# Kernel tuning notes

Measured on AMD Instinct MI355X. Metric: run time of the kernel, lower is better.

## Reference

```python
import jax, jax.numpy as jnp
import numpy as np

LN_EPS = 1e-5


def _layer_norm(x, g, b):
    mu = x.mean(-1, keepdims=True)
    var = ((x - mu) ** 2).mean(-1, keepdims=True)
    return (x - mu) / jnp.sqrt(var + LN_EPS) * g + b


def _process_memory(mem, mem_W, mem_b, ln_g, ln_b):
    # deep memory MLP: Linear -> LayerNorm -> SiLU per layer (dropout = identity in eval)
    h = mem
    for i in range(mem_W.shape[0]):
        h = jax.nn.silu(_layer_norm(h @ mem_W[i] + mem_b[i], ln_g[i], ln_b[i]))
    return h


def setup_inputs() -> dict:
    key = jax.random.key(0)
    B, S, D, M, L = 32, 2048, 1024, 1024, 2
    ks = jax.random.split(key, 12)
    s = 0.02
    inp = {
        'inputs': jax.random.normal(ks[0], (B, S, D), dtype=jnp.float32),
        'memory_state': jnp.zeros((B, M), dtype=jnp.float32),
        'momentum_state': jnp.zeros((B, M), dtype=jnp.float32),
        # projections (stored [in, out], equivalent to torch Linear weight.T)
        'Wk': jax.random.normal(ks[1], (D, M)) * s, 'bk': jnp.zeros((M,)),
        'Wv': jax.random.normal(ks[2], (D, M)) * s, 'bv': jnp.zeros((M,)),
        # deep memory layers, stacked over num_layers
        'mem_W': jax.random.normal(ks[3], (L, M, M)) * s,
        'mem_b': jnp.zeros((L, M)),
        'ln_g': jnp.ones((L, M)),
        'ln_b': jnp.zeros((L, M)),
        # gates: in = D + M
        'Wf': jax.random.normal(ks[4], (D + M, M)) * s, 'bf': jnp.zeros((M,)),
        'Wm': jax.random.normal(ks[5], (D + M, M)) * s, 'bm': jnp.zeros((M,)),
        'Wu': jax.random.normal(ks[6], (D + M, M)) * s, 'bu': jnp.zeros((M,)),
        'eta': jnp.ones((1,)) * 0.9,
        'theta': jnp.ones((1,)) * 0.1,
    }
    return inp


def reference(inputs, memory_state, momentum_state, Wk, bk, Wv, bv,
              mem_W, mem_b, ln_g, ln_b, Wf, bf, Wm, bm, Wu, bu, eta, theta):
    keys = inputs @ Wk + bk      # [B,S,M]
    values = inputs @ Wv + bv    # [B,S,M]

    def assoc_loss(mem):
        mo = _process_memory(mem, mem_W, mem_b, ln_g, ln_b)      # [B,M]
        pred = jnp.einsum('bsm,bm->bs', keys, mo)                # bmm(keys, mo^T)
        diff = pred[..., None] - values                          # expand to [B,S,M]
        return 0.5 * jnp.mean(diff ** 2)

    surprise_grad = jax.grad(assoc_loss)(memory_state)           # [B,M]

    pooled = inputs.mean(axis=1)                                 # [B,D]
    gate_in = jnp.concatenate([pooled, memory_state], axis=-1)   # [B,D+M]
    forget_g = jax.nn.sigmoid(gate_in @ Wf + bf)
    update_g = jax.nn.sigmoid(gate_in @ Wu + bu)
    # momentum_gate computed in source but unused in the update
    _ = jax.nn.sigmoid(gate_in @ Wm + bm)

    new_momentum = eta * momentum_state + theta * surprise_grad
    new_memory = (1.0 - forget_g) * memory_state + update_g * new_momentum

    processed = _process_memory(new_memory, mem_W, mem_b, ln_g, ln_b)
    return processed, jax.lax.stop_gradient(new_memory)
```

## Files before the change

kernel.cpp:

```cpp
#include <hip/hip_runtime.h>
#include <math.h>

#define Bc 32
#define Sc 2048
#define Dc 1024
#define Mc 1024
#define LNEPS 1e-5f
#define SCv (1.f/67108864.f)

typedef float f32x4 __attribute__((ext_vector_type(4)));

__device__ __forceinline__ float4 f4add(float4 a, float4 b) {
    return make_float4(a.x + b.x, a.y + b.y, a.z + b.z, a.w + b.w);
}

__device__ __forceinline__ void dreduce(float& a, float& b, float* sm) {
#pragma unroll
    for (int o = 32; o; o >>= 1) { a += __shfl_xor(a, o); b += __shfl_xor(b, o); }
    int w = threadIdx.x >> 6;
    if ((threadIdx.x & 63) == 0) { sm[w] = a; sm[4 + w] = b; }
    __syncthreads();
    a = sm[0] + sm[1] + sm[2] + sm[3];
    b = sm[4] + sm[5] + sm[6] + sm[7];
    __syncthreads();
}

__device__ __forceinline__ void wreduce(float& a, float& b) {
#pragma unroll
    for (int o = 32; o; o >>= 1) { a += __shfl_xor(a, o); b += __shfl_xor(b, o); }
}

__device__ __forceinline__ void nt_map(int t, int& n0i, int& b0i, int& ks) {
    int xcd = t & 7, rest = t >> 3;
    b0i = rest & 3;
    int q = rest >> 2;
    int s = q * 8 + xcd;
    ks = s >> 4; n0i = s & 15;
}
__device__ __forceinline__ void t_map(int t, int& dc, int& b, int& mc) {
    int xcd = t & 7, rest = t >> 3;
    b = rest & 31;
    int q = rest >> 5;
    int s = q * 8 + xcd;
    dc = s >> 3; mc = s & 7;
}

__device__ __forceinline__ void load_A128(float* Atile, const float* A, int b0, int k0) {
    for (int i = threadIdx.x; i < 1024; i += 256) {
        int r = i >> 7, c = i & 127;
        Atile[i] = A[(size_t)(b0 + r) * 1024 + k0 + c];
    }
}

__device__ __forceinline__ void nt_inner128v(const float* Atile, const float* W, int k0, int n0,
                                             float* P, int ks, int b0) {
    int lane = threadIdx.x & 63, bl = threadIdx.x >> 6;
    int n4 = lane & 15, kg = lane >> 4;
    const float* a0 = Atile + bl * 128;
    const float* a1 = Atile + (bl + 4) * 128;
    const float4* Wp = (const float4*)(W + (size_t)k0 * 1024 + n0);
    float4 acc0 = make_float4(0.f, 0.f, 0.f, 0.f);
    float4 acc1 = make_float4(0.f, 0.f, 0.f, 0.f);
#pragma unroll 8
    for (int i = 0; i < 32; ++i) {
        int k = i * 4 + kg;
        float4 w4 = Wp[(size_t)k * 256 + n4];
        float av0 = a0[k], av1 = a1[k];
        acc0.x = fmaf(av0, w4.x, acc0.x); acc0.y = fmaf(av0, w4.y, acc0.y);
        acc0.z = fmaf(av0, w4.z, acc0.z); acc0.w = fmaf(av0, w4.w, acc0.w);
        acc1.x = fmaf(av1, w4.x, acc1.x); acc1.y = fmaf(av1, w4.y, acc1.y);
        acc1.z = fmaf(av1, w4.z, acc1.z); acc1.w = fmaf(av1, w4.w, acc1.w);
    }
#pragma unroll
    for (int o = 16; o <= 32; o <<= 1) {
        acc0.x += __shfl_xor(acc0.x, o); acc0.y += __shfl_xor(acc0.y, o);
        acc0.z += __shfl_xor(acc0.z, o); acc0.w += __shfl_xor(acc0.w, o);
        acc1.x += __shfl_xor(acc1.x, o); acc1.y += __shfl_xor(acc1.y, o);
        acc1.z += __shfl_xor(acc1.z, o); acc1.w += __shfl_xor(acc1.w, o);
    }
    if (kg == 0) {
        size_t base = (size_t)ks * 32768 + n0 + 4 * n4;
        *(float4*)&P[base + (size_t)(b0 + bl) * 1024] = acc0;
        *(float4*)&P[base + (size_t)(b0 + bl + 4) * 1024] = acc1;
    }
}

__device__ __forceinline__ void t_inner(const float* Asl, const float* W,
                                        int dbase, int m0, float* outp) {
    int lane = threadIdx.x & 63, wv = threadIdx.x >> 6;
    int half = lane >> 5, m4 = lane & 31;
    float4 a4 = ((const float4*)Asl)[m4];
    int d0 = dbase + wv * 64 + half;
    float res = 0.f;
#pragma unroll 8
    for (int p = 0; p < 32; ++p) {
        int d = d0 + p * 2;
        float4 w4 = ((const float4*)(W + (size_t)d * 1024 + m0))[m4];
        float v = w4.x * a4.x + w4.y * a4.y + w4.z * a4.z + w4.w * a4.w;
#pragma unroll
        for (int o = 1; o < 32; o <<= 1) v += __shfl_xor(v, o);
        res = (m4 == p) ? v : res;
    }
    outp[wv * 64 + m4 * 2 + half] = res;
}

__global__ __launch_bounds__(256) void k_front(const float* __restrict__ Wv, const float* __restrict__ bv,
                        const float* __restrict__ mem, const float* __restrict__ W0,
                        float* __restrict__ wv_row, float* __restrict__ bvsum,
                        float* __restrict__ P1a) {
    __shared__ float shm[1032];
    int bid = blockIdx.x, tid = threadIdx.x;
    if (bid < 256) {
        float s1 = 0.f, s2 = 0.f, s3 = 0.f, s4 = 0.f;
        for (int m = tid; m < 1024; m += 256) {
            s1 += Wv[(size_t)bid * 1024 + m];
            s2 += Wv[(size_t)(bid + 256) * 1024 + m];
            s3 += Wv[(size_t)(bid + 512) * 1024 + m];
            s4 += Wv[(size_t)(bid + 768) * 1024 + m];
        }
        dreduce(s1, s2, shm + 1024);
        dreduce(s3, s4, shm + 1024);
        if (tid == 0) {
            wv_row[bid] = s1; wv_row[bid + 256] = s2;
            wv_row[bid + 512] = s3; wv_row[bid + 768] = s4;
        }
        if (bid == 0) {
            float v = 0.f, d2 = 0.f;
            for (int m = tid; m < 1024; m += 256) v += bv[m];
            dreduce(v, d2, shm + 1024);
            if (tid == 0) *bvsum = v;
        }
    } else {
        int n0i, b0i, ks;
        nt_map(bid - 256, n0i, b0i, ks);
        int n0 = n0i * 64, b0 = b0i * 8, k0 = ks * 128;
        load_A128(shm, mem, b0, k0);
        __syncthreads();
        nt_inner128v(shm, W0, k0, n0, P1a, ks, b0);
    }
}

__global__ __launch_bounds__(256) void k_gemm_ln(const float* __restrict__ P, const float* __restrict__ bias,
                          const float* __restrict__ g, const float* __restrict__ be,
                          const float* __restrict__ W1, float* __restrict__ Pout) {
    __shared__ float shm[1040];
    int tid = threadIdx.x;
    int n0i, b0i, ks;
    nt_map(blockIdx.x, n0i, b0i, ks);
    int n0 = n0i * 64, b0 = b0i * 8, k0 = ks * 128;
    float* Atile = shm; float* stats = shm + 1024;
    int wv = tid >> 6, lane = tid & 63;
    const float4* b4 = (const float4*)bias;
    for (int rr = 0; rr < 2; ++rr) {
        int r = wv + rr * 4, b = b0 + r;
        float s = 0.f, sq = 0.f;
#pragma unroll
        for (int q = 0; q < 4; ++q) {
            int m4 = lane + 64 * q;
            float4 z4 = b4[m4];
#pragma unroll
            for (int k2 = 0; k2 < 8; ++k2) {
                float4 v = ((const float4*)(P + (size_t)k2 * 32768 + (size_t)b * 1024))[m4];
                z4 = f4add(z4, v);
            }
            int c0 = 4 * m4 - k0;
            if ((unsigned)c0 < 128u) *(float4*)(Atile + r * 128 + c0) = z4;
            s += z4.x + z4.y + z4.z + z4.w;
            sq += z4.x * z4.x + z4.y * z4.y + z4.z * z4.z + z4.w * z4.w;
        }
        wreduce(s, sq);
        if (lane == 0) {
            float mean = s * (1.f / 1024.f);
            stats[r] = mean;
            stats[8 + r] = rsqrtf(sq * (1.f / 1024.f) - mean * mean + LNEPS);
        }
    }
    __syncthreads();
    for (int i = tid; i < 1024; i += 256) {
        int r = i >> 7, c = i & 127, m = k0 + c;
        float xh = (Atile[i] - stats[r]) * stats[8 + r];
        float y = fmaf(xh, g[m], be[m]);
        float sg = 1.f / (1.f + __expf(-y));
        Atile[i] = y * sg;
    }
    __syncthreads();
    nt_inner128v(Atile, W1, k0, n0, Pout, ks, b0);
}

__global__ __launch_bounds__(256) void k_wpart(const float* __restrict__ P2a, const float* __restrict__ memb1,
                        const float* __restrict__ lng1, const float* __restrict__ lnb1,
                        const float* __restrict__ bk, const float* __restrict__ Wk,
                        float* __restrict__ wpart, float* __restrict__ cbpart) {
    __shared__ float shm[136];
    int tid = threadIdx.x;
    int dc, b, mc;
    t_map(blockIdx.x, dc, b, mc);
    int m0 = mc * 128;
    float* red = shm + 128;
    float4 z4 = ((const float4*)memb1)[tid];
#pragma unroll
    for (int k2 = 0; k2 < 8; ++k2) {
        float4 v = ((const float4*)(P2a + (size_t)k2 * 32768 + (size_t)b * 1024))[tid];
        z4 = f4add(z4, v);
    }
    float s = z4.x + z4.y + z4.z + z4.w;
    float sq = z4.x * z4.x + z4.y * z4.y + z4.z * z4.z + z4.w * z4.w;
    int c0 = 4 * tid - m0;
    if ((unsigned)c0 < 128u) *(float4*)(shm + c0) = z4;
    dreduce(s, sq, red);
    float mean = s * (1.f / 1024.f);
    float rstd = rsqrtf(sq * (1.f / 1024.f) - mean * mean + LNEPS);
    if (tid < 128) {
        int m = m0 + tid;
        float xh = (shm[tid] - mean) * rstd;
        float y = fmaf(xh, lng1[m], lnb1[m]);
        float sg = 1.f / (1.f + __expf(-y));
        shm[tid] = y * sg;
    }
    __syncthreads();
    if (dc == 0) {
        float c = (tid < 128) ? bk[m0 + tid] * shm[tid] : 0.f;
        float d2 = 0.f;
        dreduce(c, d2, red);
        if (tid == 0) cbpart[mc * 32 + b] = c;
    }
    t_inner(shm, Wk, dc * 256, m0, wpart + (size_t)(mc * 32 + b) * 1024 + dc * 256);
}

__global__ __launch_bounds__(256) void k_bigpass(const float* __restrict__ X, const float* __restrict__ wpart,
                          const float* __restrict__ wv_row, const float* __restrict__ cbpart,
                          const float* __restrict__ bvsum,
                          float* __restrict__ t_part, float* __restrict__ p_part,
                          float* __restrict__ rs_part) {
    __shared__ float red[4][1024];
    __shared__ float rsum_s[4];
    int b = blockIdx.y, ch = blockIdx.x;
    int wv = threadIdx.x >> 6, lane = threadIdx.x & 63;
    float4 wreg[4], tacc[4], pacc[4];
    const float4* wp4 = (const float4*)wpart;
    const float4* wr4 = (const float4*)wv_row;
#pragma unroll
    for (int j = 0; j < 4; ++j) {
        int d4 = lane + 64 * j;
        float4 a = make_float4(0.f, 0.f, 0.f, 0.f);
#pragma unroll
        for (int mc = 0; mc < 8; ++mc) a = f4add(a, wp4[(size_t)(mc * 32 + b) * 256 + d4]);
        float4 wr = wr4[d4];
        wreg[j].x = 1024.f * a.x - wr.x;
        wreg[j].y = 1024.f * a.y - wr.y;
        wreg[j].z = 1024.f * a.z - wr.z;
        wreg[j].w = 1024.f * a.w - wr.w;
        tacc[j] = make_float4(0.f, 0.f, 0.f, 0.f);
        pacc[j] = make_float4(0.f, 0.f, 0.f, 0.f);
    }
    float cbs = 0.f;
#pragma unroll
    for (int mc = 0; mc < 8; ++mc) cbs += cbpart[mc * 32 + b];
    float cbv = 1024.f * cbs - *bvsum;
    float rloc = 0.f;
    int s0r = ch * 64 + wv * 16;
#pragma unroll 2
    for (int i = 0; i < 16; ++i) {
        const f32x4* xr = (const f32x4*)(X + ((size_t)b * Sc + s0r + i) * Dc);
        f32x4 x[4]; float pp = 0.f;
#pragma unroll
        for (int j = 0; j < 4; ++j) {
            x[j] = __builtin_nontemporal_load(xr + lane + 64 * j);
            pp += x[j].x * wreg[j].x + x[j].y * wreg[j].y + x[j].z * wreg[j].z + x[j].w * wreg[j].w;
        }
#pragma unroll
        for (int o = 32; o; o >>= 1) pp += __shfl_xor(pp, o);
        float r = pp + cbv;
        rloc += r;
#pragma unroll
        for (int j = 0; j < 4; ++j) {
            tacc[j].x = fmaf(x[j].x, r, tacc[j].x);
            tacc[j].y = fmaf(x[j].y, r, tacc[j].y);
            tacc[j].z = fmaf(x[j].z, r, tacc[j].z);
            tacc[j].w = fmaf(x[j].w, r, tacc[j].w);
            pacc[j].x += x[j].x; pacc[j].y += x[j].y;
            pacc[j].z += x[j].z; pacc[j].w += x[j].w;
        }
    }
    float4* redv = (float4*)red[wv];
#pragma unroll
    for (int j = 0; j < 4; ++j) redv[lane + 64 * j] = tacc[j];
    if (lane == 0) rsum_s[wv] = rloc;
    __syncthreads();
    size_t pb = ((size_t)b * 32 + ch) * 1024;
    for (int j = 0; j < 4; ++j) {
        int d = threadIdx.x + 256 * j;
        t_part[pb + d] = red[0][d] + red[1][d] + red[2][d] + red[3][d];
    }
    if (threadIdx.x == 0) rs_part[b * 32 + ch] = rsum_s[0] + rsum_s[1] + rsum_s[2] + rsum_s[3];
    __syncthreads();
#pragma unroll
    for (int j = 0; j < 4; ++j) redv[lane + 64 * j] = pacc[j];
    __syncthreads();
    for (int j = 0; j < 4; ++j) {
        int d = threadIdx.x + 256 * j;
        p_part[pb + d] = red[0][d] + red[1][d] + red[2][d] + red[3][d];
    }
}

__global__ __launch_bounds__(256) void k_reduce(const float* __restrict__ t_part, const float* __restrict__ p_part,
                         const float* __restrict__ rs_part,
                         float* __restrict__ tbuf, float* __restrict__ pooled,
                         float* __restrict__ rsv) {
    int idx = blockIdx.x * 256 + threadIdx.x;
    int b = idx >> 8, d4 = idx & 255;
    const float4* tp = (const float4*)t_part + (size_t)b * 8192 + d4;
    const float4* pp = (const float4*)p_part + (size_t)b * 8192 + d4;
    float4 st = make_float4(0.f, 0.f, 0.f, 0.f);
    float4 sp = make_float4(0.f, 0.f, 0.f, 0.f);
#pragma unroll 8
    for (int ch = 0; ch < 32; ++ch) {
        st = f4add(st, tp[(size_t)ch * 256]);
        sp = f4add(sp, pp[(size_t)ch * 256]);
    }
    ((float4*)tbuf)[idx] = st;
    sp.x *= (1.f / 2048.f); sp.y *= (1.f / 2048.f);
    sp.z *= (1.f / 2048.f); sp.w *= (1.f / 2048.f);
    ((float4*)pooled)[idx] = sp;
    if (blockIdx.x == 0 && threadIdx.x < 32) {
        float s = 0.f;
        for (int ch = 0; ch < 32; ++ch) s += rs_part[threadIdx.x * 32 + ch];
        rsv[threadIdx.x] = s;
    }
}

__global__ __launch_bounds__(256) void k_gates(const float* __restrict__ tbuf, const float* __restrict__ pooled,
                        const float* __restrict__ mem,
                        const float* __restrict__ Wk, const float* __restrict__ Wf,
                        const float* __restrict__ Wu,
                        float* __restrict__ Pg, float* __restrict__ Pfp, float* __restrict__ Pup,
                        float* __restrict__ Pfm, float* __restrict__ Pum) {
    __shared__ float Atile[1024];
    int bid = blockIdx.x;
    int z = bid >> 9;
    int n0i, b0i, ks;
    nt_map(bid & 511, n0i, b0i, ks);
    int n0 = n0i * 64, b0 = b0i * 8, k0 = ks * 128;
    const float* A; const float* W; float* P;
    if (z == 0)      { A = tbuf;   W = Wk;                          P = Pg; }
    else if (z == 1) { A = pooled; W = Wf;                          P = Pfp; }
    else if (z == 2) { A = pooled; W = Wu;                          P = Pup; }
    else if (z == 3) { A = mem;    W = Wf + (size_t)1024 * 1024;    P = Pfm; }
    else             { A = mem;    W = Wu + (size_t)1024 * 1024;    P = Pum; }
    load_A128(Atile, A, b0, k0);
    __syncthreads();
    nt_inner128v(Atile, W, k0, n0, P, ks, b0);
}

__global__ __launch_bounds__(256) void k_lnbwd_gemmT(const float* __restrict__ Pz, const float* __restrict__ bias,
                              const float* __restrict__ g, const float* __restrict__ be,
                              const float* __restrict__ Pgrad, int mode,
                              const float* __restrict__ bk, const float* __restrict__ rsv,
                              const float* __restrict__ W, float* __restrict__ Pout) {
    __shared__ float shm[392];
    int tid = threadIdx.x;
    int dc, b, mc;
    t_map(blockIdx.x, dc, b, mc);
    int m0 = mc * 128;
    float* red = shm + 384;
    float rsb = mode ? rsv[b] : 0.f;
    float4 z4 = ((const float4*)bias)[tid];
#pragma unroll
    for (int k2 = 0; k2 < 8; ++k2) {
        float4 v = ((const float4*)(Pz + (size_t)k2 * 32768 + (size_t)b * 1024))[tid];
        z4 = f4add(z4, v);
    }
    float s = z4.x + z4.y + z4.z + z4.w;
    float sq = z4.x * z4.x + z4.y * z4.y + z4.z * z4.z + z4.w * z4.w;
    dreduce(s, sq, red);
    float mean = s * (1.f / 1024.f);
    float rstd = rsqrtf(sq * (1.f / 1024.f) - mean * mean + LNEPS);
    float4 g4 = make_float4(0.f, 0.f, 0.f, 0.f);
#pragma unroll
    for (int k2 = 0; k2 < 8; ++k2) {
        float4 v = ((const float4*)(Pgrad + (size_t)k2 * 32768 + (size_t)b * 1024))[tid];
        g4 = f4add(g4, v);
    }
    if (mode) {
        float4 bk4 = ((const float4*)bk)[tid];
        g4.x = SCv * (g4.x + bk4.x * rsb);
        g4.y = SCv * (g4.y + bk4.y * rsb);
        g4.z = SCv * (g4.z + bk4.z * rsb);
        g4.w = SCv * (g4.w + bk4.w * rsb);
    }
    float4 gg = ((const float4*)g)[tid], bb = ((const float4*)be)[tid];
    float sa = 0.f, sax = 0.f;
    float4 a4, xh4;
    {
        xh4.x = (z4.x - mean) * rstd;
        float y = fmaf(xh4.x, gg.x, bb.x);
        float sg2 = 1.f / (1.f + __expf(-y));
        a4.x = g4.x * (sg2 * (1.f + y * (1.f - sg2))) * gg.x;
        sa += a4.x; sax += a4.x * xh4.x;
        xh4.y = (z4.y - mean) * rstd;
        y = fmaf(xh4.y, gg.y, bb.y);
        sg2 = 1.f / (1.f + __expf(-y));
        a4.y = g4.y * (sg2 * (1.f + y * (1.f - sg2))) * gg.y;
        sa += a4.y; sax += a4.y * xh4.y;
        xh4.z = (z4.z - mean) * rstd;
        y = fmaf(xh4.z, gg.z, bb.z);
        sg2 = 1.f / (1.f + __expf(-y));
        a4.z = g4.z * (sg2 * (1.f + y * (1.f - sg2))) * gg.z;
        sa += a4.z; sax += a4.z * xh4.z;
        xh4.w = (z4.w - mean) * rstd;
        y = fmaf(xh4.w, gg.w, bb.w);
        sg2 = 1.f / (1.f + __expf(-y));
        a4.w = g4.w * (sg2 * (1.f + y * (1.f - sg2))) * gg.w;
        sa += a4.w; sax += a4.w * xh4.w;
    }
    int c0 = 4 * tid - m0;
    if ((unsigned)c0 < 128u) {
        *(float4*)(shm + c0) = a4;
        *(float4*)(shm + 128 + c0) = xh4;
    }
    dreduce(sa, sax, red);
    float ma = sa * (1.f / 1024.f), mx = sax * (1.f / 1024.f);
    if (tid < 128) shm[256 + tid] = rstd * (shm[tid] - ma - shm[128 + tid] * mx);
    __syncthreads();
    t_inner(shm + 256, W, dc * 256, m0, Pout + (size_t)(mc * 32 + b) * 1024 + dc * 256);
}

__global__ __launch_bounds__(256) void k_upd_g3(const float* __restrict__ Pfm, const float* __restrict__ Pfp,
                         const float* __restrict__ Pum, const float* __restrict__ Pup,
                         const float* __restrict__ surp,
                         const float* __restrict__ bf, const float* __restrict__ bu,
                         const float* __restrict__ mem, const float* __restrict__ mom,
                         const float* __restrict__ eta, const float* __restrict__ theta,
                         const float* __restrict__ W0, float* __restrict__ P3a,
                         float* __restrict__ out_nm) {
    __shared__ float Atile[1024];
    int tid = threadIdx.x;
    int n0i, b0i, ks;
    nt_map(blockIdx.x, n0i, b0i, ks);
    int n0 = n0i * 64, b0 = b0i * 8, k0 = ks * 128;
    float etav = eta[0], thv = theta[0];
    int r = tid >> 5, c4 = tid & 31, b = b0 + r;
    int m4 = (k0 >> 2) + c4;
    float4 zf = ((const float4*)bf)[m4];
    float4 zu = ((const float4*)bu)[m4];
    float4 sv = make_float4(0.f, 0.f, 0.f, 0.f);
#pragma unroll
    for (int k2 = 0; k2 < 8; ++k2) {
        size_t ob4 = (size_t)k2 * 8192 + (size_t)b * 256 + m4;
        zf = f4add(zf, f4add(((const float4*)Pfm)[ob4], ((const float4*)Pfp)[ob4]));
        zu = f4add(zu, f4add(((const float4*)Pum)[ob4], ((const float4*)Pup)[ob4]));
        sv = f4add(sv, ((const float4*)surp)[ob4]);
    }
    float4 me = ((const float4*)mem)[(size_t)b * 256 + m4];
    float4 mo = ((const float4*)mom)[(size_t)b * 256 + m4];
    float4 nm;
    {
        float f = 1.f / (1.f + __expf(-zf.x)), u = 1.f / (1.f + __expf(-zu.x));
        nm.x = (1.f - f) * me.x + u * (etav * mo.x + thv * sv.x);
        f = 1.f / (1.f + __expf(-zf.y)); u = 1.f / (1.f + __expf(-zu.y));
        nm.y = (1.f - f) * me.y + u * (etav * mo.y + thv * sv.y);
        f = 1.f / (1.f + __expf(-zf.z)); u = 1.f / (1.f + __expf(-zu.z));
        nm.z = (1.f - f) * me.z + u * (etav * mo.z + thv * sv.z);
        f = 1.f / (1.f + __expf(-zf.w)); u = 1.f / (1.f + __expf(-zu.w));
        nm.w = (1.f - f) * me.w + u * (etav * mo.w + thv * sv.w);
    }
    *(float4*)(Atile + r * 128 + 4 * c4) = nm;
    if (n0i == 0) ((float4*)out_nm)[(size_t)b * 256 + m4] = nm;
    __syncthreads();
    nt_inner128v(Atile, W0, k0, n0, P3a, ks, b0);
}

__global__ __launch_bounds__(256) void k_final(const float* __restrict__ P4a, const float* __restrict__ memb1,
                        const float* __restrict__ lng1, const float* __restrict__ lnb1,
                        float* __restrict__ out) {
    __shared__ float sm[8];
    int b = blockIdx.x, tid = threadIdx.x;
    float4 z4 = ((const float4*)memb1)[tid];
#pragma unroll
    for (int k2 = 0; k2 < 8; ++k2) {
        float4 v = ((const float4*)(P4a + (size_t)k2 * 32768 + (size_t)b * 1024))[tid];
        z4 = f4add(z4, v);
    }
    float s = z4.x + z4.y + z4.z + z4.w;
    float sq = z4.x * z4.x + z4.y * z4.y + z4.z * z4.z + z4.w * z4.w;
    dreduce(s, sq, sm);
    float mean = s * (1.f / 1024.f);
    float rstd = rsqrtf(sq * (1.f / 1024.f) - mean * mean + LNEPS);
    float4 gg = ((const float4*)lng1)[tid], bb = ((const float4*)lnb1)[tid];
    float4 o;
    {
        float xh = (z4.x - mean) * rstd, y = fmaf(xh, gg.x, bb.x);
        o.x = y / (1.f + __expf(-y));
        xh = (z4.y - mean) * rstd; y = fmaf(xh, gg.y, bb.y);
        o.y = y / (1.f + __expf(-y));
        xh = (z4.z - mean) * rstd; y = fmaf(xh, gg.z, bb.z);
        o.z = y / (1.f + __expf(-y));
        xh = (z4.w - mean) * rstd; y = fmaf(xh, gg.w, bb.w);
        o.w = y / (1.f + __expf(-y));
    }
    ((float4*)out)[(size_t)b * 256 + tid] = o;
}

extern "C" void kernel_launch(void* const* d_in, const int* in_sizes, int n_in,
                              void* d_out, int out_size, void* d_ws, size_t ws_size,
                              hipStream_t stream) {
    const float* X    = (const float*)d_in[0];
    const float* mem  = (const float*)d_in[1];
    const float* mom  = (const float*)d_in[2];
    const float* Wk   = (const float*)d_in[3];
    const float* bk   = (const float*)d_in[4];
    const float* Wv   = (const float*)d_in[5];
    const float* bv   = (const float*)d_in[6];
    const float* memW = (const float*)d_in[7];
    const float* memb = (const float*)d_in[8];
    const float* lng  = (const float*)d_in[9];
    const float* lnb  = (const float*)d_in[10];
    const float* Wf   = (const float*)d_in[11];
    const float* bf   = (const float*)d_in[12];
    const float* Wu   = (const float*)d_in[15];
    const float* bu   = (const float*)d_in[16];
    const float* eta  = (const float*)d_in[17];
    const float* theta= (const float*)d_in[18];
    float* out = (float*)d_out;

    const size_t BM = (size_t)Bc * Mc;
    float* ws = (float*)d_ws;
    float* P1a    = ws;
    float* P2a    = ws + 8 * BM;
    float* wpart  = ws + 16 * BM;
    float* Pg     = ws + 24 * BM;
    float* Pfp    = ws + 32 * BM;
    float* Pup    = ws + 40 * BM;
    float* Pfm    = ws + 48 * BM;
    float* Pum    = ws + 56 * BM;
    float* ghp    = ws + 64 * BM;
    float* surp   = ws + 72 * BM;
    float* P3a    = ws + 80 * BM;
    float* P4a    = ws + 88 * BM;
    float* t_part = ws + 96 * BM;
    float* p_part = ws + 128 * BM;
    float* tbuf   = ws + 160 * BM;
    float* pooled = ws + 161 * BM;
    float* wv_row = ws + 162 * BM;
    float* bvsum  = wv_row + 1024;
    float* cbpart = bvsum + 1;
    float* rs_part= cbpart + 256;
    float* rsv    = rs_part + 1024;

    const float* W0 = memW;
    const float* W1 = memW + (size_t)Mc * Mc;

    k_front<<<768, 256, 0, stream>>>(Wv, bv, mem, W0, wv_row, bvsum, P1a);
    k_gemm_ln<<<512, 256, 0, stream>>>(P1a, memb, lng, lnb, W1, P2a);
    k_wpart<<<1024, 256, 0, stream>>>(P2a, memb + 1024, lng + 1024, lnb + 1024, bk, Wk, wpart, cbpart);
    k_bigpass<<<dim3(32, 32), 256, 0, stream>>>(X, wpart, wv_row, cbpart, bvsum, t_part, p_part, rs_part);
    k_reduce<<<32, 256, 0, stream>>>(t_part, p_part, rs_part, tbuf, pooled, rsv);
    k_gates<<<2560, 256, 0, stream>>>(tbuf, pooled, mem, Wk, Wf, Wu, Pg, Pfp, Pup, Pfm, Pum);
    k_lnbwd_gemmT<<<1024, 256, 0, stream>>>(P2a, memb + 1024, lng + 1024, lnb + 1024, Pg, 1, bk, rsv, W1, ghp);
    k_lnbwd_gemmT<<<1024, 256, 0, stream>>>(P1a, memb, lng, lnb, ghp, 0, bk, rsv, W0, surp);
    k_upd_g3<<<512, 256, 0, stream>>>(Pfm, Pfp, Pum, Pup, surp, bf, bu, mem, mom, eta, theta, W0, P3a, out + BM);
    k_gemm_ln<<<512, 256, 0, stream>>>(P3a, memb, lng, lnb, W1, P4a);
    k_final<<<32, 256, 0, stream>>>(P4a, memb + 1024, lng + 1024, lnb + 1024, out);
}
```

Before: 159.4 us.

## Fold reduce and final kernels into predecessors via atomic last-block counters

Removes the k_reduce and k_final launches. The last 32 blocks of k_bigpass and of the second k_gemm_ln now spin on an agent-scope atomic counter and then do the cross-block reduction and the final LayerNorm+SiLU in place. k_bigpass also gains 112 extra blocks that stream Wk, W0, W1, Wf and Wu through the cache so later kernels find them warm, and its partial-sum stores become nontemporal. The cost is spin-waiting blocks that depend on all other blocks being resident or finishing, plus extra memory traffic from the prefetch blocks competing with the main streaming pass over X.

```diff
diff --git a/kernel.cpp b/kernel.cpp
--- a/kernel.cpp
+++ b/kernel.cpp
@@ -7,6 +7,7 @@
 #define Mc 1024
 #define LNEPS 1e-5f
 #define SCv (1.f/67108864.f)
+#define AGENT __HIP_MEMORY_SCOPE_AGENT
 
 typedef float f32x4 __attribute__((ext_vector_type(4)));
 
@@ -107,9 +108,10 @@
 __global__ __launch_bounds__(256) void k_front(const float* __restrict__ Wv, const float* __restrict__ bv,
                         const float* __restrict__ mem, const float* __restrict__ W0,
                         float* __restrict__ wv_row, float* __restrict__ bvsum,
-                        float* __restrict__ P1a) {
+                        float* __restrict__ P1a, int* __restrict__ ctr) {
     __shared__ float shm[1032];
     int bid = blockIdx.x, tid = threadIdx.x;
+    if (bid == 0 && tid == 0) { ctr[0] = 0; ctr[1] = 0; }
     if (bid < 256) {
         float s1 = 0.f, s2 = 0.f, s3 = 0.f, s4 = 0.f;
         for (int m = tid; m < 1024; m += 256) {
@@ -142,8 +144,12 @@
 
 __global__ __launch_bounds__(256) void k_gemm_ln(const float* __restrict__ P, const float* __restrict__ bias,
                           const float* __restrict__ g, const float* __restrict__ be,
-                          const float* __restrict__ W1, float* __restrict__ Pout) {
+                          const float* __restrict__ W1, float* __restrict__ Pout,
+                          int* __restrict__ ctr,
+                          const float* __restrict__ memb1, const float* __restrict__ lng1,
+                          const float* __restrict__ lnb1, float* __restrict__ outF) {
     __shared__ float shm[1040];
+    __shared__ int sprev;
     int tid = threadIdx.x;
     int n0i, b0i, ks;
     nt_map(blockIdx.x, n0i, b0i, ks);
@@ -185,6 +191,47 @@
     }
     __syncthreads();
     nt_inner128v(Atile, W1, k0, n0, Pout, ks, b0);
+
+    if (ctr) {
+        __syncthreads();
+        if (tid == 0) {
+            __threadfence();
+            sprev = __hip_atomic_fetch_add(ctr, 1, __ATOMIC_ACQ_REL, AGENT);
+        }
+        __syncthreads();
+        int prev = sprev;
+        if (prev >= 480) {
+            if (tid == 0) {
+                while (__hip_atomic_load(ctr, __ATOMIC_ACQUIRE, AGENT) < 512)
+                    __builtin_amdgcn_s_sleep(4);
+            }
+            __syncthreads();
+            __threadfence();
+            int b = prev - 480;
+            float4 z4 = ((const float4*)memb1)[tid];
+#pragma unroll
+            for (int k2 = 0; k2 < 8; ++k2) {
+                float4 v = ((const float4*)(Pout + (size_t)k2 * 32768 + (size_t)b * 1024))[tid];
+                z4 = f4add(z4, v);
+            }
+            float s = z4.x + z4.y + z4.z + z4.w;
+            float sq = z4.x * z4.x + z4.y * z4.y + z4.z * z4.z + z4.w * z4.w;
+            dreduce(s, sq, shm);
+            float mean = s * (1.f / 1024.f);
+            float rstd = rsqrtf(sq * (1.f / 1024.f) - mean * mean + LNEPS);
+            float4 gg = ((const float4*)lng1)[tid], bb = ((const float4*)lnb1)[tid];
+            float4 o;
+            float xh = (z4.x - mean) * rstd, y = fmaf(xh, gg.x, bb.x);
+            o.x = y / (1.f + __expf(-y));
+            xh = (z4.y - mean) * rstd; y = fmaf(xh, gg.y, bb.y);
+            o.y = y / (1.f + __expf(-y));
+            xh = (z4.z - mean) * rstd; y = fmaf(xh, gg.z, bb.z);
+            o.z = y / (1.f + __expf(-y));
+            xh = (z4.w - mean) * rstd; y = fmaf(xh, gg.w, bb.w);
+            o.w = y / (1.f + __expf(-y));
+            ((float4*)outF)[(size_t)b * 256 + tid] = o;
+        }
+    }
 }
 
 __global__ __launch_bounds__(256) void k_wpart(const float* __restrict__ P2a, const float* __restrict__ memb1,
@@ -230,11 +277,31 @@
 __global__ __launch_bounds__(256) void k_bigpass(const float* __restrict__ X, const float* __restrict__ wpart,
                           const float* __restrict__ wv_row, const float* __restrict__ cbpart,
                           const float* __restrict__ bvsum,
+                          const float* __restrict__ Wk, const float* __restrict__ W0,
+                          const float* __restrict__ W1, const float* __restrict__ Wf,
+                          const float* __restrict__ Wu,
                           float* __restrict__ t_part, float* __restrict__ p_part,
-                          float* __restrict__ rs_part) {
+                          float* __restrict__ rs_part,
+                          float* __restrict__ tbuf, float* __restrict__ pooled,
+                          float* __restrict__ rsv, int* __restrict__ ctr) {
     __shared__ float red[4][1024];
     __shared__ float rsum_s[4];
-    int b = blockIdx.y, ch = blockIdx.x;
+    __shared__ int sprev;
+    int bid = blockIdx.x;
+    if (bid >= 1024) {
+        int wb = bid - 1024;
+        const float4* src;
+        if (wb < 16)      src = (const float4*)Wk + (size_t)wb * 16384;
+        else if (wb < 32) src = (const float4*)W1 + (size_t)(wb - 16) * 16384;
+        else if (wb < 48) src = (const float4*)W0 + (size_t)(wb - 32) * 16384;
+        else if (wb < 80) src = (const float4*)Wf + (size_t)(wb - 48) * 16384;
+        else              src = (const float4*)Wu + (size_t)(wb - 80) * 16384;
+        float4 a = make_float4(0.f, 0.f, 0.f, 0.f);
+        for (int i = threadIdx.x; i < 16384; i += 256) a = f4add(a, src[i]);
+        asm volatile("" :: "v"(a.x), "v"(a.y), "v"(a.z), "v"(a.w));
+        return;
+    }
+    int b = bid >> 5, ch = bid & 31;
     int wv = threadIdx.x >> 6, lane = threadIdx.x & 63;
     float4 wreg[4], tacc[4], pacc[4];
     const float4* wp4 = (const float4*)wpart;
@@ -290,42 +357,52 @@
     size_t pb = ((size_t)b * 32 + ch) * 1024;
     for (int j = 0; j < 4; ++j) {
         int d = threadIdx.x + 256 * j;
-        t_part[pb + d] = red[0][d] + red[1][d] + red[2][d] + red[3][d];
-    }
-    if (threadIdx.x == 0) rs_part[b * 32 + ch] = rsum_s[0] + rsum_s[1] + rsum_s[2] + rsum_s[3];
+        __builtin_nontemporal_store(red[0][d] + red[1][d] + red[2][d] + red[3][d], &t_part[pb + d]);
+    }
+    if (threadIdx.x == 0)
+        __builtin_nontemporal_store(rsum_s[0] + rsum_s[1] + rsum_s[2] + rsum_s[3], &rs_part[b * 32 + ch]);
     __syncthreads();
 #pragma unroll
     for (int j = 0; j < 4; ++j) redv[lane + 64 * j] = pacc[j];
     __syncthreads();
     for (int j = 0; j < 4; ++j) {
         int d = threadIdx.x + 256 * j;
-        p_part[pb + d] = red[0][d] + red[1][d] + red[2][d] + red[3][d];
-    }
-}
-
-__global__ __launch_bounds__(256) void k_reduce(const float* __restrict__ t_part, const float* __restrict__ p_part,
-                         const float* __restrict__ rs_part,
-                         float* __restrict__ tbuf, float* __restrict__ pooled,
-                         float* __restrict__ rsv) {
-    int idx = blockIdx.x * 256 + threadIdx.x;
-    int b = idx >> 8, d4 = idx & 255;
-    const float4* tp = (const float4*)t_part + (size_t)b * 8192 + d4;
-    const float4* pp = (const float4*)p_part + (size_t)b * 8192 + d4;
-    float4 st = make_float4(0.f, 0.f, 0.f, 0.f);
-    float4 sp = make_float4(0.f, 0.f, 0.f, 0.f);
+        __builtin_nontemporal_store(red[0][d] + red[1][d] + red[2][d] + red[3][d], &p_part[pb + d]);
+    }
+    __syncthreads();
+    if (threadIdx.x == 0) {
+        __threadfence();
+        sprev = __hip_atomic_fetch_add(ctr, 1, __ATOMIC_ACQ_REL, AGENT);
+    }
+    __syncthreads();
+    int prev = sprev;
+    if (prev >= 992) {
+        if (threadIdx.x == 0) {
+            while (__hip_atomic_load(ctr, __ATOMIC_ACQUIRE, AGENT) < 1024)
+                __builtin_amdgcn_s_sleep(4);
+        }
+        __syncthreads();
+        __threadfence();
+        int br = prev - 992;
+        int d4 = threadIdx.x;
+        const float4* tp = (const float4*)t_part + (size_t)br * 8192 + d4;
+        const float4* pp = (const float4*)p_part + (size_t)br * 8192 + d4;
+        float4 st = make_float4(0.f, 0.f, 0.f, 0.f);
+        float4 sp = make_float4(0.f, 0.f, 0.f, 0.f);
 #pragma unroll 8
-    for (int ch = 0; ch < 32; ++ch) {
-        st = f4add(st, tp[(size_t)ch * 256]);
-        sp = f4add(sp, pp[(size_t)ch * 256]);
-    }
-    ((float4*)tbuf)[idx] = st;
-    sp.x *= (1.f / 2048.f); sp.y *= (1.f / 2048.f);
-    sp.z *= (1.f / 2048.f); sp.w *= (1.f / 2048.f);
-    ((float4*)pooled)[idx] = sp;
-    if (blockIdx.x == 0 && threadIdx.x < 32) {
-        float s = 0.f;
-        for (int ch = 0; ch < 32; ++ch) s += rs_part[threadIdx.x * 32 + ch];
-        rsv[threadIdx.x] = s;
+        for (int c2 = 0; c2 < 32; ++c2) {
+            st = f4add(st, tp[(size_t)c2 * 256]);
+            sp = f4add(sp, pp[(size_t)c2 * 256]);
+        }
+        ((float4*)tbuf)[br * 256 + d4] = st;
+        sp.x *= (1.f / 2048.f); sp.y *= (1.f / 2048.f);
+        sp.z *= (1.f / 2048.f); sp.w *= (1.f / 2048.f);
+        ((float4*)pooled)[br * 256 + d4] = sp;
+        if (threadIdx.x == 0) {
+            float s = 0.f;
+            for (int c2 = 0; c2 < 32; ++c2) s += rs_part[br * 32 + c2];
+            rsv[br] = s;
+        }
     }
 }
 
@@ -470,37 +547,6 @@
     nt_inner128v(Atile, W0, k0, n0, P3a, ks, b0);
 }
 
-__global__ __launch_bounds__(256) void k_final(const float* __restrict__ P4a, const float* __restrict__ memb1,
-                        const float* __restrict__ lng1, const float* __restrict__ lnb1,
-                        float* __restrict__ out) {
-    __shared__ float sm[8];
-    int b = blockIdx.x, tid = threadIdx.x;
-    float4 z4 = ((const float4*)memb1)[tid];
-#pragma unroll
-    for (int k2 = 0; k2 < 8; ++k2) {
-        float4 v = ((const float4*)(P4a + (size_t)k2 * 32768 + (size_t)b * 1024))[tid];
-        z4 = f4add(z4, v);
-    }
-    float s = z4.x + z4.y + z4.z + z4.w;
-    float sq = z4.x * z4.x + z4.y * z4.y + z4.z * z4.z + z4.w * z4.w;
-    dreduce(s, sq, sm);
-    float mean = s * (1.f / 1024.f);
-    float rstd = rsqrtf(sq * (1.f / 1024.f) - mean * mean + LNEPS);
-    float4 gg = ((const float4*)lng1)[tid], bb = ((const float4*)lnb1)[tid];
-    float4 o;
-    {
-        float xh = (z4.x - mean) * rstd, y = fmaf(xh, gg.x, bb.x);
-        o.x = y / (1.f + __expf(-y));
-        xh = (z4.y - mean) * rstd; y = fmaf(xh, gg.y, bb.y);
-        o.y = y / (1.f + __expf(-y));
-        xh = (z4.z - mean) * rstd; y = fmaf(xh, gg.z, bb.z);
-        o.z = y / (1.f + __expf(-y));
-        xh = (z4.w - mean) * rstd; y = fmaf(xh, gg.w, bb.w);
-        o.w = y / (1.f + __expf(-y));
-    }
-    ((float4*)out)[(size_t)b * 256 + tid] = o;
-}
-
 extern "C" void kernel_launch(void* const* d_in, const int* in_sizes, int n_in,
                               void* d_out, int out_size, void* d_ws, size_t ws_size,
                               hipStream_t stream) {
@@ -546,19 +592,22 @@
     float* cbpart = bvsum + 1;
     float* rs_part= cbpart + 256;
     float* rsv    = rs_part + 1024;
+    int*   ctr    = (int*)(rsv + 32);
 
     const float* W0 = memW;
     const float* W1 = memW + (size_t)Mc * Mc;
 
-    k_front<<<768, 256, 0, stream>>>(Wv, bv, mem, W0, wv_row, bvsum, P1a);
-    k_gemm_ln<<<512, 256, 0, stream>>>(P1a, memb, lng, lnb, W1, P2a);
+    k_front<<<768, 256, 0, stream>>>(Wv, bv, mem, W0, wv_row, bvsum, P1a, ctr);
+    k_gemm_ln<<<512, 256, 0, stream>>>(P1a, memb, lng, lnb, W1, P2a,
+                                       nullptr, nullptr, nullptr, nullptr, nullptr);
     k_wpart<<<1024, 256, 0, stream>>>(P2a, memb + 1024, lng + 1024, lnb + 1024, bk, Wk, wpart, cbpart);
-    k_bigpass<<<dim3(32, 32), 256, 0, stream>>>(X, wpart, wv_row, cbpart, bvsum, t_part, p_part, rs_part);
-    k_reduce<<<32, 256, 0, stream>>>(t_part, p_part, rs_part, tbuf, pooled, rsv);
+    k_bigpass<<<1136, 256, 0, stream>>>(X, wpart, wv_row, cbpart, bvsum,
+                                        Wk, W0, W1, Wf, Wu,
+                                        t_part, p_part, rs_part, tbuf, pooled, rsv, ctr);
     k_gates<<<2560, 256, 0, stream>>>(tbuf, pooled, mem, Wk, Wf, Wu, Pg, Pfp, Pup, Pfm, Pum);
     k_lnbwd_gemmT<<<1024, 256, 0, stream>>>(P2a, memb + 1024, lng + 1024, lnb + 1024, Pg, 1, bk, rsv, W1, ghp);
     k_lnbwd_gemmT<<<1024, 256, 0, stream>>>(P1a, memb, lng, lnb, ghp, 0, bk, rsv, W0, surp);
     k_upd_g3<<<512, 256, 0, stream>>>(Pfm, Pfp, Pum, Pup, surp, bf, bu, mem, mom, eta, theta, W0, P3a, out + BM);
-    k_gemm_ln<<<512, 256, 0, stream>>>(P3a, memb, lng, lnb, W1, P4a);
-    k_final<<<32, 256, 0, stream>>>(P4a, memb + 1024, lng + 1024, lnb + 1024, out);
-}
+    k_gemm_ln<<<512, 256, 0, stream>>>(P3a, memb, lng, lnb, W1, P4a,
+                                       ctr + 1, memb + 1024, lng + 1024, lnb + 1024, out);
+}
```

New measurement: 295.6 us. 85.5% more time.
